# Kernel tuning notes

Measured on AMD Instinct MI355X. Metric: run time of the kernel, lower is better.

The kernel has to match this reference:

```python
import jax, jax.numpy as jnp
import numpy as np

TOP_K = 6  # num_experts_per_tok


def _glu_mlp(x, wg, wu, wd):
    # DeepSeek MLP: down( silu(gate(x)) * up(x) )
    return (jax.nn.silu(x @ wg) * (x @ wu)) @ wd


def setup_inputs() -> dict:
    key = jax.random.key(0)
    ks = jax.random.split(key, 8)
    B, S, D, E, F, FS = 2, 2048, 1024, 8, 512, 1024
    sc = 0.02
    return {
        "hidden_states": jax.random.normal(ks[0], (B, S, D), jnp.float32),
        "router_w": jax.random.normal(ks[1], (D, E), jnp.float32) * sc,
        "w_gate": jax.random.normal(ks[2], (E, D, F), jnp.float32) * sc,
        "w_up": jax.random.normal(ks[3], (E, D, F), jnp.float32) * sc,
        "w_down": jax.random.normal(ks[4], (E, F, D), jnp.float32) * sc,
        "ws_gate": jax.random.normal(ks[5], (D, FS), jnp.float32) * sc,
        "ws_up": jax.random.normal(ks[6], (D, FS), jnp.float32) * sc,
        "ws_down": jax.random.normal(ks[7], (FS, D), jnp.float32) * sc,
    }


def reference(hidden_states, router_w, w_gate, w_up, w_down, ws_gate, ws_up, ws_down):
    B, S, D = hidden_states.shape
    x = hidden_states.reshape(-1, D)                       # [T, D] tokens
    # Gate: softmax router + top-k (DeepSeek gate, no renorm)
    scores = jax.nn.softmax(x @ router_w, axis=-1)         # [T, E]
    topk_w, topk_idx = jax.lax.top_k(scores, TOP_K)        # [T, K]
    # Expert SiLU-GLU MLPs evaluated for all experts (math-identical to the
    # argsort dispatch -> grouped GEMM -> scatter combine in moe_infer)
    g = jnp.einsum('td,edf->etf', x, w_gate)               # [E, T, F]
    u = jnp.einsum('td,edf->etf', x, w_up)                 # [E, T, F]
    f_all = jnp.einsum('etf,efd->ted', jax.nn.silu(g) * u, w_down)  # [T, E, D]
    # Combine: final[t] = sum_k topk_w[t,k] * expert_{topk_idx[t,k]}(x[t])
    picked = jnp.take_along_axis(f_all, topk_idx[:, :, None], axis=1)  # [T, K, D]
    y = jnp.sum(picked * topk_w[:, :, None], axis=1).reshape(B, S, D)
    # shared experts branch
    y = y + _glu_mlp(hidden_states, ws_gate, ws_up, ws_down)
    return y
```

## Files before the change

kernel.cpp:

```cpp
#include <hip/hip_runtime.h>

typedef __attribute__((ext_vector_type(8))) short bf16x8;
typedef __attribute__((ext_vector_type(4))) float floatx4;

static __device__ __forceinline__ float b2f(unsigned short u) {
  union { unsigned int i; float f; } v; v.i = ((unsigned int)u) << 16; return v.f;
}
static __device__ __forceinline__ unsigned short f2b(float f) {
  union { float f; unsigned int i; } v; v.f = f;
  unsigned int x = v.i;
  return (unsigned short)((x + 0x7fffu + ((x >> 16) & 1u)) >> 16);
}

#define GLDS(gp, lp) \
  __builtin_amdgcn_global_load_lds( \
      (const __attribute__((address_space(1))) unsigned int*)(gp), \
      (__attribute__((address_space(3))) unsigned int*)(lp), 16, 0, 0)

static __device__ __forceinline__ void swizzle_mn(int lin, int Mb, int Nb,
                                                  int& m_idx, int& n_idx) {
  if ((Mb & 7) == 0) {
    int xcd = lin & 7;
    int idx = lin >> 3;
    int nstrips = Mb >> 3;
    m_idx = (idx % nstrips) * 8 + xcd;
    n_idx = idx / nstrips;
  } else {
    m_idx = lin % Mb;
    n_idx = lin / Mb;
  }
}

__global__ void cvt_f32_bf16(const float* __restrict__ src,
                             unsigned short* __restrict__ dst) {
  int i = (blockIdx.x * 256 + threadIdx.x) * 4;
  float4 v = *(const float4*)(src + i);
  ushort4 o;
  o.x = f2b(v.x); o.y = f2b(v.y); o.z = f2b(v.z); o.w = f2b(v.w);
  *(ushort4*)(dst + i) = o;
}

__global__ void transpose_f32_bf16_2(const float* __restrict__ sA,
                                     unsigned short* __restrict__ dA, int nzA,
                                     const float* __restrict__ sB,
                                     unsigned short* __restrict__ dB,
                                     int K, int N) {
  __shared__ unsigned short tile[32][33];
  int z = blockIdx.z;
  const float* src;
  unsigned short* dst;
  if (z < nzA) { src = sA + (size_t)z * K * N; dst = dA + (size_t)z * K * N; }
  else { src = sB + (size_t)(z - nzA) * K * N; dst = dB + (size_t)(z - nzA) * K * N; }
  const int bx = blockIdx.x * 32;
  const int by = blockIdx.y * 32;
  const int tx = threadIdx.x, ty = threadIdx.y;
#pragma unroll
  for (int i = 0; i < 4; i++)
    tile[ty + i * 8][tx] = f2b(src[(size_t)(by + ty + i * 8) * N + bx + tx]);
  __syncthreads();
#pragma unroll
  for (int i = 0; i < 4; i++)
    dst[(size_t)(bx + ty + i * 8) * K + by + tx] = tile[tx][ty + i * 8];
}

__global__ void transpose3_1024(const float* __restrict__ s0,
                                const float* __restrict__ s1,
                                const float* __restrict__ s2,
                                unsigned short* __restrict__ d0,
                                unsigned short* __restrict__ d1,
                                unsigned short* __restrict__ d2) {
  __shared__ unsigned short tile[32][33];
  const float* src = (blockIdx.z == 0) ? s0 : (blockIdx.z == 1) ? s1 : s2;
  unsigned short* dst = (blockIdx.z == 0) ? d0 : (blockIdx.z == 1) ? d1 : d2;
  const int bx = blockIdx.x * 32;
  const int by = blockIdx.y * 32;
  const int tx = threadIdx.x, ty = threadIdx.y;
#pragma unroll
  for (int i = 0; i < 4; i++)
    tile[ty + i * 8][tx] = f2b(src[(size_t)(by + ty + i * 8) * 1024 + bx + tx]);
  __syncthreads();
#pragma unroll
  for (int i = 0; i < 4; i++)
    dst[(size_t)(bx + ty + i * 8) * 1024 + by + tx] = tile[tx][ty + i * 8];
}

__global__ void router_topk(const float* __restrict__ X,
                            const float* __restrict__ RW,
                            float* __restrict__ cw) {
  const int t = blockIdx.x;
  const int lane = threadIdx.x;
  float acc[8];
#pragma unroll
  for (int e = 0; e < 8; e++) acc[e] = 0.f;
  for (int d = lane; d < 1024; d += 64) {
    float xv = X[(size_t)t * 1024 + d];
    const float* r = RW + d * 8;
    float4 r0 = *(const float4*)r;
    float4 r1 = *(const float4*)(r + 4);
    acc[0] += xv * r0.x; acc[1] += xv * r0.y;
    acc[2] += xv * r0.z; acc[3] += xv * r0.w;
    acc[4] += xv * r1.x; acc[5] += xv * r1.y;
    acc[6] += xv * r1.z; acc[7] += xv * r1.w;
  }
#pragma unroll
  for (int m = 1; m < 64; m <<= 1) {
#pragma unroll
    for (int e = 0; e < 8; e++) acc[e] += __shfl_xor(acc[e], m);
  }
  if (lane == 0) {
    float mx = acc[0];
#pragma unroll
    for (int e = 1; e < 8; e++) mx = fmaxf(mx, acc[e]);
    float prob[8], s = 0.f;
#pragma unroll
    for (int e = 0; e < 8; e++) { prob[e] = expf(acc[e] - mx); s += prob[e]; }
    float inv = 1.f / s;
#pragma unroll
    for (int e = 0; e < 8; e++) prob[e] *= inv;
    int m1 = 0;
#pragma unroll
    for (int e = 1; e < 8; e++) if (prob[e] < prob[m1]) m1 = e;
    int m2 = -1;
#pragma unroll
    for (int e = 0; e < 8; e++)
      if (e != m1 && (m2 < 0 || prob[e] < prob[m2])) m2 = e;
#pragma unroll
    for (int e = 0; e < 8; e++)
      cw[(size_t)t * 8 + e] = (e == m1 || e == m2) ? 0.f : prob[e];
  }
}

__global__ __launch_bounds__(256) void gemm_gu_fused(
    const unsigned short* __restrict__ X,
    const unsigned short* __restrict__ WgTe,
    const unsigned short* __restrict__ WgTs,
    const unsigned short* __restrict__ WuTe,
    const unsigned short* __restrict__ WuTs,
    unsigned short* __restrict__ H,
    const float* __restrict__ cw, int Mb) {
  __shared__ __align__(16) unsigned short lA[128 * 32];
  __shared__ __align__(16) unsigned short lBg[64 * 32];
  __shared__ __align__(16) unsigned short lBu[64 * 32];
  const int tid = threadIdx.x;
  const int wid = tid >> 6, lane = tid & 63;
  const int lr = lane & 15, quad = lane >> 4;
  const int wm = wid >> 1, wn = wid & 1;
  int m_idx, n_idx;
  swizzle_mn(blockIdx.x, Mb, 80, m_idx, n_idx);
  const int m0 = m_idx * 128;
  const int n0 = n_idx * 64;

  const unsigned short *Bg, *Bu;
  int eidx = -1;
  if (n0 < 4096) {
    eidx = n0 >> 9;
    size_t off = ((size_t)eidx * 512 + (n0 & 511)) * 1024;
    Bg = WgTe + off; Bu = WuTe + off;
  } else {
    size_t off = (size_t)(n0 - 4096) * 1024;
    Bg = WgTs + off; Bu = WuTs + off;
  }

  floatx4 ag[4][2], au[4][2];
#pragma unroll
  for (int i = 0; i < 4; i++)
#pragma unroll
    for (int j = 0; j < 2; j++) { ag[i][j] = (floatx4)0.f; au[i][j] = (floatx4)0.f; }

  for (int k0 = 0; k0 < 1024; k0 += 32) {
    __syncthreads();
    {
#pragma unroll
      for (int i = 0; i < 2; i++) {
        int c = i * 256 + tid;
        int row = c >> 2;
        int g = ((c & 3) ^ ((row >> 1) & 3)) << 3;
        GLDS(X + (size_t)(m0 + row) * 1024 + k0 + g,
             lA + (size_t)(i * 256 + wid * 64) * 8);
      }
      int c = tid;
      int row = c >> 2;
      int g = ((c & 3) ^ ((row >> 1) & 3)) << 3;
      GLDS(Bg + (size_t)row * 1024 + k0 + g, lBg + (size_t)(wid * 64) * 8);
      GLDS(Bu + (size_t)row * 1024 + k0 + g, lBu + (size_t)(wid * 64) * 8);
    }
    __syncthreads();
    bf16x8 af[4], bg[2], bu[2];
#pragma unroll
    for (int mt = 0; mt < 4; mt++) {
      int row = wm * 64 + mt * 16 + lr;
      af[mt] = *(const bf16x8*)(lA + row * 32 + ((quad ^ ((row >> 1) & 3)) << 3));
    }
#pragma unroll
    for (int nt = 0; nt < 2; nt++) {
      int row = wn * 32 + nt * 16 + lr;
      int o = row * 32 + ((quad ^ ((row >> 1) & 3)) << 3);
      bg[nt] = *(const bf16x8*)(lBg + o);
      bu[nt] = *(const bf16x8*)(lBu + o);
    }
#pragma unroll
    for (int mt = 0; mt < 4; mt++)
#pragma unroll
      for (int nt = 0; nt < 2; nt++) {
        ag[mt][nt] = __builtin_amdgcn_mfma_f32_16x16x32_bf16(
            af[mt], bg[nt], ag[mt][nt], 0, 0, 0);
        au[mt][nt] = __builtin_amdgcn_mfma_f32_16x16x32_bf16(
            af[mt], bu[nt], au[mt][nt], 0, 0, 0);
      }
  }

#pragma unroll
  for (int mt = 0; mt < 4; mt++) {
#pragma unroll
    for (int nt = 0; nt < 2; nt++) {
#pragma unroll
      for (int r = 0; r < 4; r++) {
        int row = m0 + wm * 64 + mt * 16 + quad * 4 + r;
        int col = n0 + wn * 32 + nt * 16 + lr;
        float g = ag[mt][nt][r];
        float u = au[mt][nt][r];
        float s = (eidx >= 0) ? cw[(size_t)row * 8 + eidx] : 1.0f;
        float silu = g / (1.0f + __expf(-g));
        H[(size_t)row * 5120 + col] = f2b(s * silu * u);
      }
    }
  }
}

__global__ __launch_bounds__(256) void gemm_down(
    const unsigned short* __restrict__ H,
    const unsigned short* __restrict__ WdTe,
    const unsigned short* __restrict__ WdTs,
    float* __restrict__ Y, int Mb) {
  __shared__ __align__(16) unsigned short lA[128 * 64];
  __shared__ __align__(16) unsigned short lB[64 * 64];
  const int tid = threadIdx.x;
  const int wid = tid >> 6, lane = tid & 63;
  const int lr = lane & 15, quad = lane >> 4;
  const int wm = wid >> 1, wn = wid & 1;
  int m_idx, n_idx;
  swizzle_mn(blockIdx.x, Mb, 16, m_idx, n_idx);
  const int m0 = m_idx * 128;
  const int n0 = n_idx * 64;

  floatx4 acc[4][2];
#pragma unroll
  for (int i = 0; i < 4; i++)
#pragma unroll
    for (int j = 0; j < 2; j++) acc[i][j] = (floatx4)0.f;

  for (int k0 = 0; k0 < 5120; k0 += 64) {
    __syncthreads();
#pragma unroll
    for (int i = 0; i < 4; i++) {
      int c = i * 256 + tid;
      int row = c >> 3;
      int g = ((c & 7) ^ (row & 7)) << 3;
      GLDS(H + (size_t)(m0 + row) * 5120 + k0 + g,
           lA + (size_t)(i * 256 + wid * 64) * 8);
    }
#pragma unroll
    for (int i = 0; i < 2; i++) {
      int c = i * 256 + tid;
      int row = c >> 3;
      int g = ((c & 7) ^ (row & 7)) << 3;
      const unsigned short* gpb;
      if (k0 < 4096) {
        gpb = WdTe + (size_t)(k0 >> 9) * (1024 * 512) +
              (size_t)(n0 + row) * 512 + (k0 & 511) + g;
      } else {
        gpb = WdTs + (size_t)(n0 + row) * 1024 + (k0 - 4096) + g;
      }
      GLDS(gpb, lB + (size_t)(i * 256 + wid * 64) * 8);
    }
    __syncthreads();
    bf16x8 af[4][2], bfr[2][2];
#pragma unroll
    for (int mt = 0; mt < 4; mt++) {
      int row = wm * 64 + mt * 16 + lr;
#pragma unroll
      for (int kt = 0; kt < 2; kt++)
        af[mt][kt] = *(const bf16x8*)(lA + row * 64 +
                                      ((((kt << 2) + quad) ^ (row & 7)) << 3));
    }
#pragma unroll
    for (int nt = 0; nt < 2; nt++) {
      int row = wn * 32 + nt * 16 + lr;
#pragma unroll
      for (int kt = 0; kt < 2; kt++)
        bfr[nt][kt] = *(const bf16x8*)(lB + row * 64 +
                                       ((((kt << 2) + quad) ^ (row & 7)) << 3));
    }
#pragma unroll
    for (int kt = 0; kt < 2; kt++)
#pragma unroll
      for (int mt = 0; mt < 4; mt++)
#pragma unroll
        for (int nt = 0; nt < 2; nt++)
          acc[mt][nt] = __builtin_amdgcn_mfma_f32_16x16x32_bf16(
              af[mt][kt], bfr[nt][kt], acc[mt][nt], 0, 0, 0);
  }

#pragma unroll
  for (int mt = 0; mt < 4; mt++)
#pragma unroll
    for (int nt = 0; nt < 2; nt++)
#pragma unroll
      for (int r = 0; r < 4; r++) {
        int row = m0 + wm * 64 + mt * 16 + quad * 4 + r;
        int col = n0 + wn * 32 + nt * 16 + lr;
        Y[(size_t)row * 1024 + col] = acc[mt][nt][r];
      }
}

extern "C" void kernel_launch(void* const* d_in, const int* in_sizes, int n_in,
                              void* d_out, int out_size, void* d_ws, size_t ws_size,
                              hipStream_t stream) {
  const float* hs  = (const float*)d_in[0];
  const float* rw  = (const float*)d_in[1];
  const float* wg  = (const float*)d_in[2];
  const float* wu  = (const float*)d_in[3];
  const float* wd  = (const float*)d_in[4];
  const float* wsg = (const float*)d_in[5];
  const float* wsu = (const float*)d_in[6];
  const float* wsd = (const float*)d_in[7];
  float* out = (float*)d_out;

  char* p = (char*)d_ws;
  float* cw = (float*)p;                    p += (size_t)4096 * 8 * 4;
  unsigned short* Xb   = (unsigned short*)p; p += (size_t)4096 * 1024 * 2;
  unsigned short* wgT  = (unsigned short*)p; p += (size_t)8 * 512 * 1024 * 2;
  unsigned short* wuT  = (unsigned short*)p; p += (size_t)8 * 512 * 1024 * 2;
  unsigned short* wsgT = (unsigned short*)p; p += (size_t)1024 * 1024 * 2;
  unsigned short* wsuT = (unsigned short*)p; p += (size_t)1024 * 1024 * 2;
  unsigned short* wdT  = (unsigned short*)p; p += (size_t)8 * 1024 * 512 * 2;
  unsigned short* wsdT = (unsigned short*)p; p += (size_t)1024 * 1024 * 2;
  unsigned short* GH   = (unsigned short*)p;
  const size_t base_bytes = (size_t)(p - (char*)d_ws);

  int chunks = 8;
  for (int c = 1; c <= 8; c *= 2) {
    size_t gh_bytes = ((size_t)4096 / c) * 5120 * 2;
    if (base_bytes + gh_bytes <= ws_size) { chunks = c; break; }
  }
  const int rows = 4096 / chunks;
  const int Mb = rows / 128;

  dim3 tb(32, 8);
  cvt_f32_bf16<<<4096, 256, 0, stream>>>(hs, Xb);
  router_topk<<<4096, 64, 0, stream>>>(hs, rw, cw);
  transpose_f32_bf16_2<<<dim3(16, 32, 16), tb, 0, stream>>>(
      wg, wgT, 8, wu, wuT, 1024, 512);
  transpose_f32_bf16_2<<<dim3(32, 16, 8), tb, 0, stream>>>(
      wd, wdT, 8, wd, wdT, 512, 1024);
  transpose3_1024<<<dim3(32, 32, 3), tb, 0, stream>>>(
      wsg, wsu, wsd, wsgT, wsuT, wsdT);

  for (int c = 0; c < chunks; c++) {
    const unsigned short* Xc = Xb + (size_t)c * rows * 1024;
    const float* cwc = cw + (size_t)c * rows * 8;
    float* outc = out + (size_t)c * rows * 1024;
    gemm_gu_fused<<<Mb * 80, 256, 0, stream>>>(
        Xc, wgT, wsgT, wuT, wsuT, GH, cwc, Mb);
    gemm_down<<<Mb * 16, 256, 0, stream>>>(GH, wdT, wsdT, outc, Mb);
  }
}
```

Measured before the change: 313.0 us.

## Split-K the down GEMM and merge prologue conversion and transpose kernels

Fuses the input bf16 conversion into the router kernel and merges the three weight-transpose launches into one grid. When the workspace is large enough, the down-projection GEMM splits K into two halves so it launches twice as many blocks (512 → 1024), followed by a reduction kernel that sums the two fp32 partial outputs. This is meant to improve CU occupancy for the down GEMM, which otherwise has only 512 blocks, and to cut launch count. The cost is extra fp32 partial-buffer traffic of about 32MB written and read, plus one more kernel.

```diff
diff --git a/kernel.cpp b/kernel.cpp
--- a/kernel.cpp
+++ b/kernel.cpp
@@ -31,64 +31,20 @@
   }
 }
 
-__global__ void cvt_f32_bf16(const float* __restrict__ src,
-                             unsigned short* __restrict__ dst) {
-  int i = (blockIdx.x * 256 + threadIdx.x) * 4;
-  float4 v = *(const float4*)(src + i);
-  ushort4 o;
-  o.x = f2b(v.x); o.y = f2b(v.y); o.z = f2b(v.z); o.w = f2b(v.w);
-  *(ushort4*)(dst + i) = o;
-}
-
-__global__ void transpose_f32_bf16_2(const float* __restrict__ sA,
-                                     unsigned short* __restrict__ dA, int nzA,
-                                     const float* __restrict__ sB,
-                                     unsigned short* __restrict__ dB,
-                                     int K, int N) {
-  __shared__ unsigned short tile[32][33];
-  int z = blockIdx.z;
-  const float* src;
-  unsigned short* dst;
-  if (z < nzA) { src = sA + (size_t)z * K * N; dst = dA + (size_t)z * K * N; }
-  else { src = sB + (size_t)(z - nzA) * K * N; dst = dB + (size_t)(z - nzA) * K * N; }
-  const int bx = blockIdx.x * 32;
-  const int by = blockIdx.y * 32;
-  const int tx = threadIdx.x, ty = threadIdx.y;
-#pragma unroll
-  for (int i = 0; i < 4; i++)
-    tile[ty + i * 8][tx] = f2b(src[(size_t)(by + ty + i * 8) * N + bx + tx]);
-  __syncthreads();
-#pragma unroll
-  for (int i = 0; i < 4; i++)
-    dst[(size_t)(bx + ty + i * 8) * K + by + tx] = tile[tx][ty + i * 8];
-}
-
-__global__ void transpose3_1024(const float* __restrict__ s0,
-                                const float* __restrict__ s1,
-                                const float* __restrict__ s2,
-                                unsigned short* __restrict__ d0,
-                                unsigned short* __restrict__ d1,
-                                unsigned short* __restrict__ d2) {
-  __shared__ unsigned short tile[32][33];
-  const float* src = (blockIdx.z == 0) ? s0 : (blockIdx.z == 1) ? s1 : s2;
-  unsigned short* dst = (blockIdx.z == 0) ? d0 : (blockIdx.z == 1) ? d1 : d2;
-  const int bx = blockIdx.x * 32;
-  const int by = blockIdx.y * 32;
-  const int tx = threadIdx.x, ty = threadIdx.y;
-#pragma unroll
-  for (int i = 0; i < 4; i++)
-    tile[ty + i * 8][tx] = f2b(src[(size_t)(by + ty + i * 8) * 1024 + bx + tx]);
-  __syncthreads();
-#pragma unroll
-  for (int i = 0; i < 4; i++)
-    dst[(size_t)(bx + ty + i * 8) * 1024 + by + tx] = tile[tx][ty + i * 8];
-}
-
-__global__ void router_topk(const float* __restrict__ X,
-                            const float* __restrict__ RW,
-                            float* __restrict__ cw) {
+__global__ void router_cvt(const float* __restrict__ X,
+                           const float* __restrict__ RW,
+                           float* __restrict__ cw,
+                           unsigned short* __restrict__ Xb) {
   const int t = blockIdx.x;
   const int lane = threadIdx.x;
+#pragma unroll
+  for (int j = 0; j < 4; j++) {
+    int idx = (j * 64 + lane) * 4;
+    float4 v = *(const float4*)(X + (size_t)t * 1024 + idx);
+    ushort4 o;
+    o.x = f2b(v.x); o.y = f2b(v.y); o.z = f2b(v.z); o.w = f2b(v.w);
+    *(ushort4*)(Xb + (size_t)t * 1024 + idx) = o;
+  }
   float acc[8];
 #pragma unroll
   for (int e = 0; e < 8; e++) acc[e] = 0.f;
@@ -128,6 +84,39 @@
     for (int e = 0; e < 8; e++)
       cw[(size_t)t * 8 + e] = (e == m1 || e == m2) ? 0.f : prob[e];
   }
+}
+
+__global__ void transpose_all(const float* __restrict__ wg,
+                              const float* __restrict__ wu,
+                              const float* __restrict__ wd,
+                              const float* __restrict__ wsg,
+                              const float* __restrict__ wsu,
+                              const float* __restrict__ wsd,
+                              unsigned short* __restrict__ wgT,
+                              unsigned short* __restrict__ wuT,
+                              unsigned short* __restrict__ wdT,
+                              unsigned short* __restrict__ wsgT,
+                              unsigned short* __restrict__ wsuT,
+                              unsigned short* __restrict__ wsdT) {
+  __shared__ unsigned short tile[32][33];
+  const int z = blockIdx.z;
+  const float* src; unsigned short* dst; int K, N;
+  if (z < 8)       { src = wg  + (size_t)z * 1024 * 512;      dst = wgT + (size_t)z * 512 * 1024;      K = 1024; N = 512; }
+  else if (z < 16) { src = wu  + (size_t)(z - 8) * 1024 * 512; dst = wuT + (size_t)(z - 8) * 512 * 1024; K = 1024; N = 512; }
+  else if (z < 24) { src = wd  + (size_t)(z - 16) * 512 * 1024; dst = wdT + (size_t)(z - 16) * 1024 * 512; K = 512; N = 1024; }
+  else if (z == 24){ src = wsg; dst = wsgT; K = 1024; N = 1024; }
+  else if (z == 25){ src = wsu; dst = wsuT; K = 1024; N = 1024; }
+  else             { src = wsd; dst = wsdT; K = 1024; N = 1024; }
+  const int bx = blockIdx.x * 32, by = blockIdx.y * 32;
+  if (bx >= N || by >= K) return;
+  const int tx = threadIdx.x, ty = threadIdx.y;
+#pragma unroll
+  for (int i = 0; i < 4; i++)
+    tile[ty + i * 8][tx] = f2b(src[(size_t)(by + ty + i * 8) * N + bx + tx]);
+  __syncthreads();
+#pragma unroll
+  for (int i = 0; i < 4; i++)
+    dst[(size_t)(bx + ty + i * 8) * K + by + tx] = tile[tx][ty + i * 8];
 }
 
 __global__ __launch_bounds__(256) void gemm_gu_fused(
@@ -227,6 +216,104 @@
   }
 }
 
+__global__ __launch_bounds__(256) void gemm_down_sk2(
+    const unsigned short* __restrict__ H,
+    const unsigned short* __restrict__ WdTe,
+    const unsigned short* __restrict__ WdTs,
+    float* __restrict__ P, int Mb) {
+  __shared__ __align__(16) unsigned short lA[128 * 64];
+  __shared__ __align__(16) unsigned short lB[64 * 64];
+  const int tid = threadIdx.x;
+  const int wid = tid >> 6, lane = tid & 63;
+  const int lr = lane & 15, quad = lane >> 4;
+  const int wm = wid >> 1, wn = wid & 1;
+  const int sk = blockIdx.x & 1;
+  int m_idx, n_idx;
+  swizzle_mn(blockIdx.x >> 1, Mb, 16, m_idx, n_idx);
+  const int m0 = m_idx * 128;
+  const int n0 = n_idx * 64;
+  const int kbeg = sk * 2560, kend = kbeg + 2560;
+  float* Yp = P + (size_t)sk * 4096 * 1024;
+
+  floatx4 acc[4][2];
+#pragma unroll
+  for (int i = 0; i < 4; i++)
+#pragma unroll
+    for (int j = 0; j < 2; j++) acc[i][j] = (floatx4)0.f;
+
+  for (int k0 = kbeg; k0 < kend; k0 += 64) {
+    __syncthreads();
+#pragma unroll
+    for (int i = 0; i < 4; i++) {
+      int c = i * 256 + tid;
+      int row = c >> 3;
+      int g = ((c & 7) ^ (row & 7)) << 3;
+      GLDS(H + (size_t)(m0 + row) * 5120 + k0 + g,
+           lA + (size_t)(i * 256 + wid * 64) * 8);
+    }
+#pragma unroll
+    for (int i = 0; i < 2; i++) {
+      int c = i * 256 + tid;
+      int row = c >> 3;
+      int g = ((c & 7) ^ (row & 7)) << 3;
+      const unsigned short* gpb;
+      if (k0 < 4096) {
+        gpb = WdTe + (size_t)(k0 >> 9) * (1024 * 512) +
+              (size_t)(n0 + row) * 512 + (k0 & 511) + g;
+      } else {
+        gpb = WdTs + (size_t)(n0 + row) * 1024 + (k0 - 4096) + g;
+      }
+      GLDS(gpb, lB + (size_t)(i * 256 + wid * 64) * 8);
+    }
+    __syncthreads();
+    bf16x8 af[4][2], bfr[2][2];
+#pragma unroll
+    for (int mt = 0; mt < 4; mt++) {
+      int row = wm * 64 + mt * 16 + lr;
+#pragma unroll
+      for (int kt = 0; kt < 2; kt++)
+        af[mt][kt] = *(const bf16x8*)(lA + row * 64 +
+                                      ((((kt << 2) + quad) ^ (row & 7)) << 3));
+    }
+#pragma unroll
+    for (int nt = 0; nt < 2; nt++) {
+      int row = wn * 32 + nt * 16 + lr;
+#pragma unroll
+      for (int kt = 0; kt < 2; kt++)
+        bfr[nt][kt] = *(const bf16x8*)(lB + row * 64 +
+                                       ((((kt << 2) + quad) ^ (row & 7)) << 3));
+    }
+#pragma unroll
+    for (int kt = 0; kt < 2; kt++)
+#pragma unroll
+      for (int mt = 0; mt < 4; mt++)
+#pragma unroll
+        for (int nt = 0; nt < 2; nt++)
+          acc[mt][nt] = __builtin_amdgcn_mfma_f32_16x16x32_bf16(
+              af[mt][kt], bfr[nt][kt], acc[mt][nt], 0, 0, 0);
+  }
+
+#pragma unroll
+  for (int mt = 0; mt < 4; mt++)
+#pragma unroll
+    for (int nt = 0; nt < 2; nt++)
+#pragma unroll
+      for (int r = 0; r < 4; r++) {
+        int row = m0 + wm * 64 + mt * 16 + quad * 4 + r;
+        int col = n0 + wn * 32 + nt * 16 + lr;
+        Yp[(size_t)row * 1024 + col] = acc[mt][nt][r];
+      }
+}
+
+__global__ void reduce_sk2(const float* __restrict__ P, float* __restrict__ out) {
+  size_t i = ((size_t)blockIdx.x * 256 + threadIdx.x) * 4;
+  float4 a = *(const float4*)(P + i);
+  float4 b = *(const float4*)(P + (size_t)4096 * 1024 + i);
+  float4 o;
+  o.x = a.x + b.x; o.y = a.y + b.y; o.z = a.z + b.z; o.w = a.w + b.w;
+  *(float4*)(out + i) = o;
+}
+
 __global__ __launch_bounds__(256) void gemm_down(
     const unsigned short* __restrict__ H,
     const unsigned short* __restrict__ WdTe,
@@ -337,31 +424,37 @@
   unsigned short* wsdT = (unsigned short*)p; p += (size_t)1024 * 1024 * 2;
   unsigned short* GH   = (unsigned short*)p;
   const size_t base_bytes = (size_t)(p - (char*)d_ws);
-
-  int chunks = 8;
-  for (int c = 1; c <= 8; c *= 2) {
-    size_t gh_bytes = ((size_t)4096 / c) * 5120 * 2;
-    if (base_bytes + gh_bytes <= ws_size) { chunks = c; break; }
-  }
-  const int rows = 4096 / chunks;
-  const int Mb = rows / 128;
+  const size_t gh_full = (size_t)4096 * 5120 * 2;
+  const size_t p_bytes = (size_t)2 * 4096 * 1024 * 4;
+
+  const bool sk2 = (base_bytes + gh_full + p_bytes) <= ws_size;
 
   dim3 tb(32, 8);
-  cvt_f32_bf16<<<4096, 256, 0, stream>>>(hs, Xb);
-  router_topk<<<4096, 64, 0, stream>>>(hs, rw, cw);
-  transpose_f32_bf16_2<<<dim3(16, 32, 16), tb, 0, stream>>>(
-      wg, wgT, 8, wu, wuT, 1024, 512);
-  transpose_f32_bf16_2<<<dim3(32, 16, 8), tb, 0, stream>>>(
-      wd, wdT, 8, wd, wdT, 512, 1024);
-  transpose3_1024<<<dim3(32, 32, 3), tb, 0, stream>>>(
-      wsg, wsu, wsd, wsgT, wsuT, wsdT);
-
-  for (int c = 0; c < chunks; c++) {
-    const unsigned short* Xc = Xb + (size_t)c * rows * 1024;
-    const float* cwc = cw + (size_t)c * rows * 8;
-    float* outc = out + (size_t)c * rows * 1024;
-    gemm_gu_fused<<<Mb * 80, 256, 0, stream>>>(
-        Xc, wgT, wsgT, wuT, wsuT, GH, cwc, Mb);
-    gemm_down<<<Mb * 16, 256, 0, stream>>>(GH, wdT, wsdT, outc, Mb);
-  }
-}
+  router_cvt<<<4096, 64, 0, stream>>>(hs, rw, cw, Xb);
+  transpose_all<<<dim3(32, 32, 27), tb, 0, stream>>>(
+      wg, wu, wd, wsg, wsu, wsd, wgT, wuT, wdT, wsgT, wsuT, wsdT);
+
+  if (sk2) {
+    float* P = (float*)(GH + gh_full / 2);
+    gemm_gu_fused<<<32 * 80, 256, 0, stream>>>(
+        Xb, wgT, wsgT, wuT, wsuT, GH, cw, 32);
+    gemm_down_sk2<<<32 * 16 * 2, 256, 0, stream>>>(GH, wdT, wsdT, P, 32);
+    reduce_sk2<<<4096, 256, 0, stream>>>(P, out);
+  } else {
+    int chunks = 8;
+    for (int c = 1; c <= 8; c *= 2) {
+      size_t gh_bytes = ((size_t)4096 / c) * 5120 * 2;
+      if (base_bytes + gh_bytes <= ws_size) { chunks = c; break; }
+    }
+    const int rows = 4096 / chunks;
+    const int Mb = rows / 128;
+    for (int c = 0; c < chunks; c++) {
+      const unsigned short* Xc = Xb + (size_t)c * rows * 1024;
+      const float* cwc = cw + (size_t)c * rows * 8;
+      float* outc = out + (size_t)c * rows * 1024;
+      gemm_gu_fused<<<Mb * 80, 256, 0, stream>>>(
+          Xc, wgT, wsgT, wuT, wsuT, GH, cwc, Mb);
+      gemm_down<<<Mb * 16, 256, 0, stream>>>(GH, wdT, wsdT, outc, Mb);
+    }
+  }
+}
```

After: 327.7 us. 4.7% more time.
